# Performance work log

Measured on AMD Instinct MI355X. Metric: run time of the kernel, lower is better.

## Reference

```python
import jax, jax.numpy as jnp
import numpy as np

H, KVH, D = 32, 8, 128          # query heads, kv heads, head dim
HID = H * D                      # 4096
N_REP = H // KVH
HEAVY_RATIO, RECENT_RATIO = 0.1, 0.1
B, S = 1, 2048


def setup_inputs() -> dict:
    key = jax.random.key(0)
    ks = jax.random.split(key, 8)
    scale = 0.02
    hidden_states = jax.random.normal(ks[0], (B, S, HID), jnp.float32)
    neg = jnp.finfo(jnp.float32).min
    causal = jnp.where(jnp.tril(jnp.ones((S, S), bool)), 0.0, neg)
    attention_mask = jnp.broadcast_to(causal[None, None], (B, 1, S, S)).astype(jnp.float32)
    return {
        "hidden_states": hidden_states,
        "attention_mask": attention_mask,
        "Wq": jax.random.normal(ks[1], (HID, H * D), jnp.float32) * scale,
        "bq": jax.random.normal(ks[2], (H * D,), jnp.float32) * scale,
        "Wk": jax.random.normal(ks[3], (HID, KVH * D), jnp.float32) * scale,
        "bk": jax.random.normal(ks[4], (KVH * D,), jnp.float32) * scale,
        "Wv": jax.random.normal(ks[5], (HID, KVH * D), jnp.float32) * scale,
        "bv": jax.random.normal(ks[6], (KVH * D,), jnp.float32) * scale,
        "Wo": jax.random.normal(ks[7], (H * D, HID), jnp.float32) * scale,
    }


def reference(hidden_states, attention_mask, Wq, bq, Wk, bk, Wv, bv, Wo):
    b, s, _ = hidden_states.shape
    # QKV projections (q/k/v have bias, o does not)
    q = (hidden_states @ Wq + bq).reshape(b, s, H, D).transpose(0, 2, 1, 3)      # [B,H,S,D]
    k = (hidden_states @ Wk + bk).reshape(b, s, KVH, D).transpose(0, 2, 1, 3)    # [B,KVH,S,D]
    v = (hidden_states @ Wv + bv).reshape(b, s, KVH, D).transpose(0, 2, 1, 3)
    # repeat_kv: head h uses kv head h // N_REP (matches expand+reshape order)
    k = jnp.repeat(k, N_REP, axis=1)                                             # [B,H,S,D]
    v = jnp.repeat(v, N_REP, axis=1)
    scores = jnp.einsum('bhqd,bhkd->bhqk', q, k) / jnp.sqrt(jnp.asarray(D, q.dtype))
    neg = jnp.finfo(scores.dtype).min
    scores = jnp.maximum(scores + attention_mask, neg)
    attn = jax.nn.softmax(scores.astype(jnp.float32), axis=-1).astype(q.dtype)   # [B,H,S,S]
    # H2O: accumulate per-key scores (first step: no previous_scores)
    cur_scores = attn.sum(axis=0).sum(axis=1)                                    # [H, S]
    heavy_budget = int(HEAVY_RATIO * s)
    recent_budget = int(RECENT_RATIO * s)
    # cache_budget = heavy + recent < s, so eviction branch always runs here
    mask = jnp.ones((H, s + 1), attn.dtype)
    mask = mask.at[:, : s + 1 - recent_budget].set(0.0)
    selected = cur_scores[:, : s - recent_budget]                                # exclude recent window
    _, topk_idx = jax.lax.top_k(selected, heavy_budget)                          # [H, heavy]
    mask = jax.vmap(lambda m, i: m.at[i].set(1.0))(mask, topk_idx)               # scatter heavy hitters
    attention_masks_next = mask[None, :, None, :]                                # [1,H,1,S+1]
    score_mask = mask[:, :-1].at[:, -recent_budget:].set(1.0)
    new_scores = cur_scores * score_mask                                         # evicted scores zeroed
    # attention output
    out = jnp.einsum('bhqk,bhkd->bhqd', attn, v)                                 # [B,H,S,D]
    out = out.transpose(0, 2, 1, 3).reshape(b, s, HID) @ Wo
    return out, attention_masks_next, new_scores
```

## Files before the change

### kernel.cpp

```cpp
#include <hip/hip_runtime.h>
#include <stdint.h>

#define SEQ 2048
#define HID 4096
#define KVHID 1024
#define NHEAD 32
#define DHEAD 128
#define HEAVY 204
#define SEL_N 1844

typedef float f32x4 __attribute__((ext_vector_type(4)));
typedef __bf16 bf16x8 __attribute__((ext_vector_type(8)));

#define MFMA16 __builtin_amdgcn_mfma_f32_16x16x32_bf16

__device__ __forceinline__ unsigned short f2bf(float x) {
    unsigned int u = __float_as_uint(x);
    u = (u + 0x7fffu + ((u >> 16) & 1u)) >> 16;
    return (unsigned short)u;
}
__device__ __forceinline__ float bf2f(unsigned short s) {
    return __uint_as_float(((unsigned int)s) << 16);
}
__device__ __forceinline__ unsigned long long pack4(unsigned short a, unsigned short b,
                                                    unsigned short c, unsigned short d) {
    return (unsigned long long)a | ((unsigned long long)b << 16) |
           ((unsigned long long)c << 32) | ((unsigned long long)d << 48);
}
__device__ __forceinline__ float fexp2(float x) {
#if __has_builtin(__builtin_amdgcn_exp2f)
    return __builtin_amdgcn_exp2f(x);
#else
    float r; asm volatile("v_exp_f32 %0, %1\ns_nop 1" : "=v"(r) : "v"(x)); return r;
#endif
}
__device__ __forceinline__ unsigned cvt_pk_bf16(float lo, float hi) {
    unsigned r; asm("v_cvt_pk_bf16_f32 %0, %1, %2" : "=v"(r) : "v"(lo), "v"(hi)); return r;
}
__device__ __forceinline__ void gload_lds16(const unsigned short* g, unsigned short* l) {
    __builtin_amdgcn_global_load_lds(
        (const __attribute__((address_space(1))) void*)g,
        (__attribute__((address_space(3))) void*)l, 16, 0, 0);
}
__device__ __forceinline__ void block_sync() {
    asm volatile("" ::: "memory");
    __builtin_amdgcn_s_barrier();
    asm volatile("" ::: "memory");
}

__global__ __launch_bounds__(256) void split_f32(const float* __restrict__ in,
    unsigned short* __restrict__ hi, unsigned short* __restrict__ lo, int n4)
{
    int i = blockIdx.x * 256 + threadIdx.x;
    const int stride = gridDim.x * 256;
    for (; i < n4; i += stride) {
        const float4 v = ((const float4*)in)[i];
        const unsigned short h0 = f2bf(v.x), h1 = f2bf(v.y), h2 = f2bf(v.z), h3 = f2bf(v.w);
        ((unsigned long long*)hi)[i] = pack4(h0, h1, h2, h3);
        ((unsigned long long*)lo)[i] = pack4(f2bf(v.x - bf2f(h0)), f2bf(v.y - bf2f(h1)),
                                             f2bf(v.z - bf2f(h2)), f2bf(v.w - bf2f(h3)));
    }
}

template<bool SPLIT>
__global__ __launch_bounds__(256) void wprep(const float* __restrict__ W,
    unsigned short* __restrict__ Thi, unsigned short* __restrict__ Tlo, int K, int N)
{
    __shared__ float T[64][65];
    const int k0 = blockIdx.y << 6, n0 = blockIdx.x << 6;
    const int tid = threadIdx.x;
    const int c = tid & 63, r4 = tid >> 6;
    #pragma unroll
    for (int i = 0; i < 16; ++i)
        T[r4 + i * 4][c] = W[(size_t)(k0 + r4 + i * 4) * N + n0 + c];
    __syncthreads();
    #pragma unroll
    for (int i = 0; i < 16; ++i) {
        const int n = r4 + i * 4;
        const float x = T[c][n];
        const size_t o = (size_t)(n0 + n) * K + k0 + c;
        const unsigned short h = f2bf(x);
        Thi[o] = h;
        if constexpr (SPLIT) Tlo[o] = f2bf(x - bf2f(h));
    }
}

template<bool SPLIT, int OUTMODE , bool BIAS>
__global__ __launch_bounds__(256) void gemm2(
    const unsigned short* __restrict__ Ahi, const unsigned short* __restrict__ Alo,
    const unsigned short* __restrict__ Bhi, const unsigned short* __restrict__ Blo,
    const float* __restrict__ bias,
    void* __restrict__ C0, unsigned short* __restrict__ C1,
    int M, int N, int K)
{
    constexpr int NT = SPLIT ? 4 : 2;
    __shared__ unsigned short sm[2][NT][128 * 32];

    const int tid = threadIdx.x;
    const int l = tid & 63, w = tid >> 6;
    const int lr = l & 15, lg = l >> 4;
    const int wm = (w >> 1) * 64, wn = (w & 1) * 64;
    const int m0 = blockIdx.y * 128, n0 = blockIdx.x * 128;

    const unsigned short* aH = Ahi + (size_t)m0 * K;
    const unsigned short* bH = Bhi + (size_t)n0 * K;
    const unsigned short* aL = SPLIT ? Alo + (size_t)m0 * K : nullptr;
    const unsigned short* bL = SPLIT ? Blo + (size_t)n0 * K : nullptr;

    const int s0_ = tid, s1_ = tid + 256;
    const int r0_ = s0_ >> 2, c0_ = (s0_ & 3) ^ (r0_ & 3);
    const int r1_ = s1_ >> 2, c1_ = (s1_ & 3) ^ (r1_ & 3);
    const size_t g0off = (size_t)r0_ * K + c0_ * 8;
    const size_t g1off = (size_t)r1_ * K + c1_ * 8;

#define STAGE(buf, kk)                                                          \
    do {                                                                        \
        const int k0s = (kk) << 5;                                              \
        gload_lds16(aH + g0off + k0s, &sm[buf][0][s0_ * 8]);                    \
        gload_lds16(aH + g1off + k0s, &sm[buf][0][s1_ * 8]);                    \
        gload_lds16(bH + g0off + k0s, &sm[buf][1][s0_ * 8]);                    \
        gload_lds16(bH + g1off + k0s, &sm[buf][1][s1_ * 8]);                    \
        if constexpr (SPLIT) {                                                  \
            gload_lds16(aL + g0off + k0s, &sm[buf][2][s0_ * 8]);                \
            gload_lds16(aL + g1off + k0s, &sm[buf][2][s1_ * 8]);                \
            gload_lds16(bL + g0off + k0s, &sm[buf][3][s0_ * 8]);                \
            gload_lds16(bL + g1off + k0s, &sm[buf][3][s1_ * 8]);                \
        }                                                                       \
    } while (0)

    f32x4 acc[4][4];
    #pragma unroll
    for (int i = 0; i < 4; ++i)
        #pragma unroll
        for (int j = 0; j < 4; ++j) acc[i][j] = (f32x4){};

    const int nk = K >> 5;
    STAGE(0, 0);
    for (int kt = 0; kt < nk; ++kt) {
        if (kt + 1 < nk) {
            STAGE((kt + 1) & 1, kt + 1);
            if constexpr (SPLIT) asm volatile("s_waitcnt vmcnt(8)" ::: "memory");
            else                 asm volatile("s_waitcnt vmcnt(4)" ::: "memory");
        } else {
            asm volatile("s_waitcnt vmcnt(0)" ::: "memory");
        }
        block_sync();
        {
            const unsigned short (*smb)[128 * 32] = sm[kt & 1];
            bf16x8 ah[4], bh[4], al[4], bl[4];
            #pragma unroll
            for (int mi = 0; mi < 4; ++mi) {
                const int rr = wm + mi * 16 + lr;
                const int o = rr * 32 + ((lg ^ (rr & 3)) << 3);
                ah[mi] = *(const bf16x8*)(&smb[0][o]);
                if constexpr (SPLIT) al[mi] = *(const bf16x8*)(&smb[2][o]);
            }
            #pragma unroll
            for (int ni = 0; ni < 4; ++ni) {
                const int rr = wn + ni * 16 + lr;
                const int o = rr * 32 + ((lg ^ (rr & 3)) << 3);
                bh[ni] = *(const bf16x8*)(&smb[1][o]);
                if constexpr (SPLIT) bl[ni] = *(const bf16x8*)(&smb[3][o]);
            }
            #pragma unroll
            for (int mi = 0; mi < 4; ++mi)
                #pragma unroll
                for (int ni = 0; ni < 4; ++ni) {
                    acc[mi][ni] = MFMA16(ah[mi], bh[ni], acc[mi][ni], 0, 0, 0);
                    if constexpr (SPLIT) {
                        acc[mi][ni] = MFMA16(ah[mi], bl[ni], acc[mi][ni], 0, 0, 0);
                        acc[mi][ni] = MFMA16(al[mi], bh[ni], acc[mi][ni], 0, 0, 0);
                    }
                }
        }
        block_sync();
    }
#undef STAGE

    #pragma unroll
    for (int ni = 0; ni < 4; ++ni) {
        const int col = n0 + wn + ni * 16 + lr;
        float bv = 0.f;
        if constexpr (BIAS) bv = bias[col];
        #pragma unroll
        for (int mi = 0; mi < 4; ++mi) {
            #pragma unroll
            for (int r = 0; r < 4; ++r) {
                const int row = m0 + wm + mi * 16 + lg * 4 + r;
                const float x = acc[mi][ni][r] + bv;
                const size_t o = (size_t)row * N + col;
                if constexpr (OUTMODE == 1) {
                    ((float*)C0)[o] = x;
                } else if constexpr (OUTMODE == 0) {
                    ((unsigned short*)C0)[o] = f2bf(x);
                } else {
                    const unsigned short hi = f2bf(x);
                    ((unsigned short*)C0)[o] = hi;
                    C1[o] = f2bf(x - bf2f(hi));
                }
            }
        }
    }
}

__global__ __launch_bounds__(256) void transpose_v(const unsigned short* __restrict__ v,
                                                   unsigned short* __restrict__ vt)
{
    __shared__ unsigned short T[64][65];
    const int r0 = blockIdx.x * 64;
    const int c0 = blockIdx.y * 64;
    const int tid = threadIdx.x;
    const int cc = tid & 63, rr = tid >> 6;
    #pragma unroll
    for (int i = 0; i < 16; ++i)
        T[rr + i * 4][cc] = v[(size_t)(r0 + rr + i * 4) * KVHID + c0 + cc];
    __syncthreads();
    #pragma unroll
    for (int i = 0; i < 16; ++i) {
        const int oc = rr + i * 4;
        vt[(size_t)(c0 + oc) * SEQ + r0 + cc] = T[cc][oc];
    }
}

__device__ __forceinline__ void stage_tile(
    const unsigned short* __restrict__ khi, const unsigned short* __restrict__ klo,
    unsigned short* kb, int kt, int kvoff, int w, int lane)
{
    const unsigned short* src = (w >> 1) ? klo : khi;
    unsigned short* dst = kb + (w >> 1) * 4096 + (w & 1) * 2048;
    const int lsub = lane >> 4;
    const int lbyte = (lane & 15) * 16;
    #pragma unroll
    for (int j = 0; j < 4; ++j) {
        const int row = (w & 1) * 16 + j * 4 + lsub;
        const int soff = (lbyte ^ ((row & 7) << 4)) >> 1;
        const unsigned short* g = src + (size_t)(kt * 32 + row) * KVHID + kvoff + soff;
        gload_lds16(g, dst + j * 512);
    }
}

__device__ __forceinline__ void process_qblock(
    int head, int qb, int w, int lane,
    const unsigned short* __restrict__ qhi, const unsigned short* __restrict__ qlo,
    const unsigned short* __restrict__ khi, const unsigned short* __restrict__ klo,
    const unsigned short* __restrict__ vT,
    unsigned short* __restrict__ obuf, double* __restrict__ colsum,
    unsigned short* kbuf, unsigned short* pl)
{
    const int lr = lane & 15, lg = lane >> 4;
    const int kv = head >> 2;
    const int kvoff = kv * DHEAD;
    const int q0 = qb * 64;
    const int q0w = q0 + w * 16;
    const int NT = 2 * qb + 2;
    const int wnt = ((q0w + 15) >> 5) + 1;
    const float C = 0.08838834764831845f * 1.44269504088896340f;

    bf16x8 qh[4], qlo4[4];
    {
        const size_t qbase = (size_t)(q0w + lr) * HID + head * DHEAD + lg * 8;
        #pragma unroll
        for (int s = 0; s < 4; ++s) {
            qh[s]   = *(const bf16x8*)(qhi + qbase + s * 32);
            qlo4[s] = *(const bf16x8*)(qlo + qbase + s * 32);
        }
    }
    const int swz = (lr & 7) << 3;

    float rl[4];
    {
        float lp[4] = {0.f, 0.f, 0.f, 0.f};
        stage_tile(khi, klo, kbuf, 0, kvoff, w, lane);
        for (int kt = 0; kt < NT; ++kt) {
            unsigned short* kb = kbuf + (kt & 1) * 8192;
            if (kt + 1 < NT) {
                stage_tile(khi, klo, kbuf + ((kt + 1) & 1) * 8192, kt + 1, kvoff, w, lane);
                asm volatile("s_waitcnt vmcnt(4)" ::: "memory");
            } else {
                asm volatile("s_waitcnt vmcnt(0)" ::: "memory");
            }
            block_sync();
            if (kt < wnt) {
                f32x4 m0 = {}, m1 = {}, x0 = {}, x1 = {};
                #pragma unroll
                for (int s = 0; s < 4; ++s) {
                    const int d = s * 32 + lg * 8;
                    const bf16x8 k0h = *(const bf16x8*)(kb + (lr * 128 + (d ^ swz)));
                    const bf16x8 k1h = *(const bf16x8*)(kb + ((16 + lr) * 128 + (d ^ swz)));
                    const bf16x8 k0l = *(const bf16x8*)(kb + 4096 + lr * 128 + (d ^ swz));
                    const bf16x8 k1l = *(const bf16x8*)(kb + 4096 + (16 + lr) * 128 + (d ^ swz));
                    m0 = MFMA16(qh[s], k0h, m0, 0, 0, 0);
                    m1 = MFMA16(qh[s], k1h, m1, 0, 0, 0);
                    x0 = MFMA16(qlo4[s], k0h, MFMA16(qh[s], k0l, x0, 0, 0, 0), 0, 0, 0);
                    x1 = MFMA16(qlo4[s], k1h, MFMA16(qh[s], k1l, x1, 0, 0, 0), 0, 0, 0);
                }
                const bool full = (kt * 32 + 31 <= q0w);
                #pragma unroll
                for (int r = 0; r < 4; ++r) {
                    float e0 = fexp2((m0[r] + x0[r]) * C);
                    float e1 = fexp2((m1[r] + x1[r]) * C);
                    if (!full) {
                        const int q = q0w + lg * 4 + r;
                        if (kt * 32 + lr > q)      e0 = 0.f;
                        if (kt * 32 + 16 + lr > q) e1 = 0.f;
                    }
                    lp[r] += e0 + e1;
                }
            }
            block_sync();
        }
        #pragma unroll
        for (int r = 0; r < 4; ++r) {
            float v = lp[r];
            v += __shfl_xor(v, 1);
            v += __shfl_xor(v, 2);
            v += __shfl_xor(v, 4);
            v += __shfl_xor(v, 8);
            rl[r] = 1.0f / v;
        }
    }
    {
        f32x4 oacc[8];
        #pragma unroll
        for (int f = 0; f < 8; ++f) oacc[f] = (f32x4){};
        stage_tile(khi, klo, kbuf, 0, kvoff, w, lane);
        for (int kt = 0; kt < NT; ++kt) {
            unsigned short* kb = kbuf + (kt & 1) * 8192;
            if (kt + 1 < NT) {
                stage_tile(khi, klo, kbuf + ((kt + 1) & 1) * 8192, kt + 1, kvoff, w, lane);
                asm volatile("s_waitcnt vmcnt(4)" ::: "memory");
            } else {
                asm volatile("s_waitcnt vmcnt(0)" ::: "memory");
            }
            block_sync();
            if (kt < wnt) {
                f32x4 m0 = {}, m1 = {}, x0 = {}, x1 = {};
                #pragma unroll
                for (int s = 0; s < 4; ++s) {
                    const int d = s * 32 + lg * 8;
                    const bf16x8 k0h = *(const bf16x8*)(kb + (lr * 128 + (d ^ swz)));
                    const bf16x8 k1h = *(const bf16x8*)(kb + ((16 + lr) * 128 + (d ^ swz)));
                    const bf16x8 k0l = *(const bf16x8*)(kb + 4096 + lr * 128 + (d ^ swz));
                    const bf16x8 k1l = *(const bf16x8*)(kb + 4096 + (16 + lr) * 128 + (d ^ swz));
                    m0 = MFMA16(qh[s], k0h, m0, 0, 0, 0);
                    m1 = MFMA16(qh[s], k1h, m1, 0, 0, 0);
                    x0 = MFMA16(qlo4[s], k0h, MFMA16(qh[s], k0l, x0, 0, 0, 0), 0, 0, 0);
                    x1 = MFMA16(qlo4[s], k1h, MFMA16(qh[s], k1l, x1, 0, 0, 0), 0, 0, 0);
                }
                const bool full = (kt * 32 + 31 <= q0w);
                float p0[4], p1[4];
                float cs0 = 0.f, cs1 = 0.f;
                #pragma unroll
                for (int r = 0; r < 4; ++r) {
                    float e0 = fexp2((m0[r] + x0[r]) * C);
                    float e1 = fexp2((m1[r] + x1[r]) * C);
                    if (!full) {
                        const int q = q0w + lg * 4 + r;
                        if (kt * 32 + lr > q)      e0 = 0.f;
                        if (kt * 32 + 16 + lr > q) e1 = 0.f;
                    }
                    p0[r] = e0 * rl[r];
                    p1[r] = e1 * rl[r];
                    cs0 += p0[r];
                    cs1 += p1[r];
                }
                cs0 += __shfl_xor(cs0, 16); cs0 += __shfl_xor(cs0, 32);
                cs1 += __shfl_xor(cs1, 16); cs1 += __shfl_xor(cs1, 32);
                if (lg == 0) {
                    atomicAdd(&colsum[head * SEQ + kt * 32 + lr], (double)cs0);
                    atomicAdd(&colsum[head * SEQ + kt * 32 + 16 + lr], (double)cs1);
                }
                #pragma unroll
                for (int r = 0; r < 4; r += 2) {
                    const int row0 = (lg * 4 + r) * 40;
                    unsigned u0 = cvt_pk_bf16(p0[r], p0[r + 1]);
                    unsigned u1 = cvt_pk_bf16(p1[r], p1[r + 1]);
                    pl[row0 + lr]      = (unsigned short)u0;
                    pl[row0 + 40 + lr] = (unsigned short)(u0 >> 16);
                    pl[row0 + 16 + lr] = (unsigned short)u1;
                    pl[row0 + 56 + lr] = (unsigned short)(u1 >> 16);
                }
                const bf16x8 pa = *(const bf16x8*)(pl + lr * 40 + lg * 8);
                #pragma unroll
                for (int f = 0; f < 8; ++f) {
                    const bf16x8 vf = *(const bf16x8*)(vT + (size_t)(kvoff + f * 16 + lr) * SEQ
                                                       + kt * 32 + lg * 8);
                    oacc[f] = MFMA16(pa, vf, oacc[f], 0, 0, 0);
                }
            }
            block_sync();
        }
        #pragma unroll
        for (int f = 0; f < 8; ++f)
            #pragma unroll
            for (int r = 0; r < 4; ++r)
                obuf[(size_t)(q0w + lg * 4 + r) * HID + head * DHEAD + f * 16 + lr] =
                    f2bf(oacc[f][r]);
    }
}

__global__ __launch_bounds__(256, 2) void attn_fused2(
    const unsigned short* __restrict__ qhi, const unsigned short* __restrict__ qlo,
    const unsigned short* __restrict__ khi, const unsigned short* __restrict__ klo,
    const unsigned short* __restrict__ vT,
    unsigned short* __restrict__ obuf, double* __restrict__ colsum)
{
    __shared__ unsigned short kbuf[2][2 * 4096];
    __shared__ unsigned short plds[4][16 * 40];
    const int head = blockIdx.x >> 4;
    const int pr = blockIdx.x & 15;
    const int tid = threadIdx.x;
    const int w = tid >> 6, lane = tid & 63;
    process_qblock(head, pr, w, lane, qhi, qlo, khi, klo, vT, obuf, colsum,
                   &kbuf[0][0], &plds[w][0]);
    process_qblock(head, 31 - pr, w, lane, qhi, qlo, khi, klo, vT, obuf, colsum,
                   &kbuf[0][0], &plds[w][0]);
}

__global__ __launch_bounds__(256) void topk_kernel(const double* __restrict__ colsum,
                                                   float* __restrict__ outbuf)
{
    __shared__ float sc[SEL_N];
    __shared__ unsigned char fl[SEL_N];
    __shared__ int cnt;
    const int h = blockIdx.x;
    const int tid = threadIdx.x;
    for (int j = tid; j < SEL_N; j += 256) {
        sc[j] = (float)colsum[h * SEQ + j];
        fl[j] = 0;
    }
    __syncthreads();
    unsigned int cand = 0u;
    for (int b = 30; b >= 0; --b) {
        const unsigned int t = cand | (1u << b);
        const float tv = __uint_as_float(t);
        if (tid == 0) cnt = 0;
        __syncthreads();
        int local = 0;
        for (int j = tid; j < SEL_N; j += 256) local += (sc[j] >= tv) ? 1 : 0;
        atomicAdd(&cnt, local);
        __syncthreads();
        if (cnt >= HEAVY) cand = t;
        __syncthreads();
    }
    const float v204 = __uint_as_float(cand);
    if (tid == 0) cnt = 0;
    __syncthreads();
    int local = 0;
    for (int j = tid; j < SEL_N; j += 256) {
        if (sc[j] > v204) { fl[j] = 1; local++; }
    }
    atomicAdd(&cnt, local);
    __syncthreads();
    if (tid == 0) {
        int need = HEAVY - cnt;
        for (int j = 0; j < SEL_N && need > 0; ++j) {
            if (sc[j] == v204) { fl[j] = 1; --need; }
        }
    }
    __syncthreads();
    float* mask_out = outbuf + 8388608 + h * 2049;
    float* score_out = outbuf + 8388608 + NHEAD * 2049 + h * SEQ;
    for (int j = tid; j < 2049; j += 256) {
        float mv;
        if (j >= 1845) mv = 1.f;
        else if (j < SEL_N) mv = fl[j] ? 1.f : 0.f;
        else mv = 0.f;
        mask_out[j] = mv;
    }
    for (int j = tid; j < SEQ; j += 256) {
        const float cur = (float)colsum[h * SEQ + j];
        const float smv = (j >= SEL_N) ? 1.f : (fl[j] ? 1.f : 0.f);
        score_out[j] = cur * smv;
    }
}

extern "C" void kernel_launch(void* const* d_in, const int* in_sizes, int n_in,
                              void* d_out, int out_size, void* d_ws, size_t ws_size,
                              hipStream_t stream)
{
    const float* hidden = (const float*)d_in[0];
    const float* Wq = (const float*)d_in[2];
    const float* bq = (const float*)d_in[3];
    const float* Wk = (const float*)d_in[4];
    const float* bk = (const float*)d_in[5];
    const float* Wv = (const float*)d_in[6];
    const float* bv = (const float*)d_in[7];
    const float* Wo = (const float*)d_in[8];
    float* out = (float*)d_out;

    char* ws = (char*)d_ws;
    unsigned short* hs_hi = (unsigned short*)(ws);
    unsigned short* hs_lo = (unsigned short*)(ws + 16777216ull);
    unsigned short* wqT_hi = (unsigned short*)(ws + 33554432ull);
    unsigned short* wqT_lo = (unsigned short*)(ws + 67108864ull);
    unsigned short* wkT_hi = (unsigned short*)(ws + 100663296ull);
    unsigned short* wkT_lo = (unsigned short*)(ws + 109051904ull);
    unsigned short* wvT    = (unsigned short*)(ws + 117440512ull);
    unsigned short* q_hi   = (unsigned short*)(ws + 125829120ull);
    unsigned short* q_lo   = (unsigned short*)(ws + 142606336ull);
    unsigned short* k_hi   = (unsigned short*)(ws + 159383552ull);
    unsigned short* k_lo   = (unsigned short*)(ws + 163577856ull);
    unsigned short* v_bf   = (unsigned short*)(ws + 167772160ull);
    unsigned short* vT     = (unsigned short*)(ws + 171966464ull);
    unsigned short* o_bf   = (unsigned short*)(ws + 176160768ull);
    double* colsum         = (double*)(ws + 192937984ull);
    unsigned short* woT    = wqT_hi;

    dim3 blk(256);
    split_f32<<<dim3(2048), blk, 0, stream>>>(hidden, hs_hi, hs_lo, (SEQ * HID) / 4);
    wprep<true><<<dim3(64, 64), blk, 0, stream>>>(Wq, wqT_hi, wqT_lo, HID, HID);
    wprep<true><<<dim3(16, 64), blk, 0, stream>>>(Wk, wkT_hi, wkT_lo, HID, KVHID);
    wprep<false><<<dim3(16, 64), blk, 0, stream>>>(Wv, wvT, nullptr, HID, KVHID);

    gemm2<true, 2, true><<<dim3(32, 16), blk, 0, stream>>>(
        hs_hi, hs_lo, wqT_hi, wqT_lo, bq, q_hi, q_lo, SEQ, HID, HID);
    gemm2<true, 2, true><<<dim3(8, 16), blk, 0, stream>>>(
        hs_hi, hs_lo, wkT_hi, wkT_lo, bk, k_hi, k_lo, SEQ, KVHID, HID);
    gemm2<false, 0, true><<<dim3(8, 16), blk, 0, stream>>>(
        hs_hi, nullptr, wvT, nullptr, bv, v_bf, nullptr, SEQ, KVHID, HID);

    transpose_v<<<dim3(32, 16), blk, 0, stream>>>(v_bf, vT);
    (void)hipMemsetAsync((void*)colsum, 0, (size_t)NHEAD * SEQ * sizeof(double), stream);
    attn_fused2<<<dim3(512), blk, 0, stream>>>(q_hi, q_lo, k_hi, k_lo, vT, o_bf, colsum);
    topk_kernel<<<dim3(32), blk, 0, stream>>>(colsum, out);

    wprep<false><<<dim3(64, 64), blk, 0, stream>>>(Wo, woT, nullptr, HID, HID);
    gemm2<false, 1, false><<<dim3(32, 16), blk, 0, stream>>>(
        o_bf, nullptr, woT, nullptr, nullptr, out, nullptr, SEQ, HID, HID);
}
```

Measured before the change: 855.3 us.

## Split attention into one block per q-block with scrambled order and MFMA priority

The attention kernel now launches 1024 blocks, one per (head, q-block), instead of 512 blocks that each processed a paired short and long causal q-block. A hashed q-block index spreads work across CUs, and launch bounds are raised to 4 blocks per CU for higher occupancy. It also breaks the dependent MFMA chains for the hi/lo correction terms into independent accumulators and wraps MFMA sections (including the GEMM) in s_setprio. The cost is losing the explicit causal load-pairing and adding register pressure under the tighter launch bound.

```diff
diff --git a/kernel.cpp b/kernel.cpp
--- a/kernel.cpp
+++ b/kernel.cpp
@@ -162,6 +162,7 @@
                 bh[ni] = *(const bf16x8*)(&smb[1][o]);
                 if constexpr (SPLIT) bl[ni] = *(const bf16x8*)(&smb[3][o]);
             }
+            __builtin_amdgcn_s_setprio(1);
             #pragma unroll
             for (int mi = 0; mi < 4; ++mi)
                 #pragma unroll
@@ -172,6 +173,7 @@
                         acc[mi][ni] = MFMA16(al[mi], bh[ni], acc[mi][ni], 0, 0, 0);
                     }
                 }
+            __builtin_amdgcn_s_setprio(0);
         }
         block_sync();
     }
@@ -239,19 +241,23 @@
     }
 }
 
-__device__ __forceinline__ void process_qblock(
-    int head, int qb, int w, int lane,
+__global__ __launch_bounds__(256, 4) void attn_fused3(
     const unsigned short* __restrict__ qhi, const unsigned short* __restrict__ qlo,
     const unsigned short* __restrict__ khi, const unsigned short* __restrict__ klo,
     const unsigned short* __restrict__ vT,
-    unsigned short* __restrict__ obuf, double* __restrict__ colsum,
-    unsigned short* kbuf, unsigned short* pl)
-{
+    unsigned short* __restrict__ obuf, double* __restrict__ colsum)
+{
+    __shared__ unsigned short kbuf[2][2 * 4096];
+    __shared__ unsigned short plds[4][16 * 40];
+    const int head = blockIdx.x >> 5;
+    const int qb = ((blockIdx.x & 31) * 13 + head * 7) & 31;
+    const int tid = threadIdx.x;
+    const int w = tid >> 6, lane = tid & 63;
+    unsigned short* pl = &plds[w][0];
+
     const int lr = lane & 15, lg = lane >> 4;
-    const int kv = head >> 2;
-    const int kvoff = kv * DHEAD;
-    const int q0 = qb * 64;
-    const int q0w = q0 + w * 16;
+    const int kvoff = (head >> 2) * DHEAD;
+    const int q0w = qb * 64 + w * 16;
     const int NT = 2 * qb + 2;
     const int wnt = ((q0w + 15) >> 5) + 1;
     const float C = 0.08838834764831845f * 1.44269504088896340f;
@@ -270,18 +276,19 @@
     float rl[4];
     {
         float lp[4] = {0.f, 0.f, 0.f, 0.f};
-        stage_tile(khi, klo, kbuf, 0, kvoff, w, lane);
+        stage_tile(khi, klo, &kbuf[0][0], 0, kvoff, w, lane);
         for (int kt = 0; kt < NT; ++kt) {
-            unsigned short* kb = kbuf + (kt & 1) * 8192;
+            unsigned short* kb = &kbuf[kt & 1][0];
             if (kt + 1 < NT) {
-                stage_tile(khi, klo, kbuf + ((kt + 1) & 1) * 8192, kt + 1, kvoff, w, lane);
+                stage_tile(khi, klo, &kbuf[(kt + 1) & 1][0], kt + 1, kvoff, w, lane);
                 asm volatile("s_waitcnt vmcnt(4)" ::: "memory");
             } else {
                 asm volatile("s_waitcnt vmcnt(0)" ::: "memory");
             }
             block_sync();
             if (kt < wnt) {
-                f32x4 m0 = {}, m1 = {}, x0 = {}, x1 = {};
+                f32x4 m0 = {}, m1 = {}, xa0 = {}, xb0 = {}, xa1 = {}, xb1 = {};
+                __builtin_amdgcn_s_setprio(1);
                 #pragma unroll
                 for (int s = 0; s < 4; ++s) {
                     const int d = s * 32 + lg * 8;
@@ -289,16 +296,19 @@
                     const bf16x8 k1h = *(const bf16x8*)(kb + ((16 + lr) * 128 + (d ^ swz)));
                     const bf16x8 k0l = *(const bf16x8*)(kb + 4096 + lr * 128 + (d ^ swz));
                     const bf16x8 k1l = *(const bf16x8*)(kb + 4096 + (16 + lr) * 128 + (d ^ swz));
-                    m0 = MFMA16(qh[s], k0h, m0, 0, 0, 0);
-                    m1 = MFMA16(qh[s], k1h, m1, 0, 0, 0);
-                    x0 = MFMA16(qlo4[s], k0h, MFMA16(qh[s], k0l, x0, 0, 0, 0), 0, 0, 0);
-                    x1 = MFMA16(qlo4[s], k1h, MFMA16(qh[s], k1l, x1, 0, 0, 0), 0, 0, 0);
-                }
+                    m0  = MFMA16(qh[s],   k0h, m0,  0, 0, 0);
+                    m1  = MFMA16(qh[s],   k1h, m1,  0, 0, 0);
+                    xa0 = MFMA16(qh[s],   k0l, xa0, 0, 0, 0);
+                    xb0 = MFMA16(qlo4[s], k0h, xb0, 0, 0, 0);
+                    xa1 = MFMA16(qh[s],   k1l, xa1, 0, 0, 0);
+                    xb1 = MFMA16(qlo4[s], k1h, xb1, 0, 0, 0);
+                }
+                __builtin_amdgcn_s_setprio(0);
                 const bool full = (kt * 32 + 31 <= q0w);
                 #pragma unroll
                 for (int r = 0; r < 4; ++r) {
-                    float e0 = fexp2((m0[r] + x0[r]) * C);
-                    float e1 = fexp2((m1[r] + x1[r]) * C);
+                    float e0 = fexp2((m0[r] + (xa0[r] + xb0[r])) * C);
+                    float e1 = fexp2((m1[r] + (xa1[r] + xb1[r])) * C);
                     if (!full) {
                         const int q = q0w + lg * 4 + r;
                         if (kt * 32 + lr > q)      e0 = 0.f;
@@ -323,18 +333,19 @@
         f32x4 oacc[8];
         #pragma unroll
         for (int f = 0; f < 8; ++f) oacc[f] = (f32x4){};
-        stage_tile(khi, klo, kbuf, 0, kvoff, w, lane);
+        stage_tile(khi, klo, &kbuf[0][0], 0, kvoff, w, lane);
         for (int kt = 0; kt < NT; ++kt) {
-            unsigned short* kb = kbuf + (kt & 1) * 8192;
+            unsigned short* kb = &kbuf[kt & 1][0];
             if (kt + 1 < NT) {
-                stage_tile(khi, klo, kbuf + ((kt + 1) & 1) * 8192, kt + 1, kvoff, w, lane);
+                stage_tile(khi, klo, &kbuf[(kt + 1) & 1][0], kt + 1, kvoff, w, lane);
                 asm volatile("s_waitcnt vmcnt(4)" ::: "memory");
             } else {
                 asm volatile("s_waitcnt vmcnt(0)" ::: "memory");
             }
             block_sync();
             if (kt < wnt) {
-                f32x4 m0 = {}, m1 = {}, x0 = {}, x1 = {};
+                f32x4 m0 = {}, m1 = {}, xa0 = {}, xb0 = {}, xa1 = {}, xb1 = {};
+                __builtin_amdgcn_s_setprio(1);
                 #pragma unroll
                 for (int s = 0; s < 4; ++s) {
                     const int d = s * 32 + lg * 8;
@@ -342,18 +353,21 @@
                     const bf16x8 k1h = *(const bf16x8*)(kb + ((16 + lr) * 128 + (d ^ swz)));
                     const bf16x8 k0l = *(const bf16x8*)(kb + 4096 + lr * 128 + (d ^ swz));
                     const bf16x8 k1l = *(const bf16x8*)(kb + 4096 + (16 + lr) * 128 + (d ^ swz));
-                    m0 = MFMA16(qh[s], k0h, m0, 0, 0, 0);
-                    m1 = MFMA16(qh[s], k1h, m1, 0, 0, 0);
-                    x0 = MFMA16(qlo4[s], k0h, MFMA16(qh[s], k0l, x0, 0, 0, 0), 0, 0, 0);
-                    x1 = MFMA16(qlo4[s], k1h, MFMA16(qh[s], k1l, x1, 0, 0, 0), 0, 0, 0);
-                }
+                    m0  = MFMA16(qh[s],   k0h, m0,  0, 0, 0);
+                    m1  = MFMA16(qh[s],   k1h, m1,  0, 0, 0);
+                    xa0 = MFMA16(qh[s],   k0l, xa0, 0, 0, 0);
+                    xb0 = MFMA16(qlo4[s], k0h, xb0, 0, 0, 0);
+                    xa1 = MFMA16(qh[s],   k1l, xa1, 0, 0, 0);
+                    xb1 = MFMA16(qlo4[s], k1h, xb1, 0, 0, 0);
+                }
+                __builtin_amdgcn_s_setprio(0);
                 const bool full = (kt * 32 + 31 <= q0w);
                 float p0[4], p1[4];
                 float cs0 = 0.f, cs1 = 0.f;
                 #pragma unroll
                 for (int r = 0; r < 4; ++r) {
-                    float e0 = fexp2((m0[r] + x0[r]) * C);
-                    float e1 = fexp2((m1[r] + x1[r]) * C);
+                    float e0 = fexp2((m0[r] + (xa0[r] + xb0[r])) * C);
+                    float e1 = fexp2((m1[r] + (xa1[r] + xb1[r])) * C);
                     if (!full) {
                         const int q = q0w + lg * 4 + r;
                         if (kt * 32 + lr > q)      e0 = 0.f;
@@ -381,12 +395,14 @@
                     pl[row0 + 56 + lr] = (unsigned short)(u1 >> 16);
                 }
                 const bf16x8 pa = *(const bf16x8*)(pl + lr * 40 + lg * 8);
+                __builtin_amdgcn_s_setprio(1);
                 #pragma unroll
                 for (int f = 0; f < 8; ++f) {
                     const bf16x8 vf = *(const bf16x8*)(vT + (size_t)(kvoff + f * 16 + lr) * SEQ
                                                        + kt * 32 + lg * 8);
                     oacc[f] = MFMA16(pa, vf, oacc[f], 0, 0, 0);
                 }
+                __builtin_amdgcn_s_setprio(0);
             }
             block_sync();
         }
@@ -397,24 +413,6 @@
                 obuf[(size_t)(q0w + lg * 4 + r) * HID + head * DHEAD + f * 16 + lr] =
                     f2bf(oacc[f][r]);
     }
-}
-
-__global__ __launch_bounds__(256, 2) void attn_fused2(
-    const unsigned short* __restrict__ qhi, const unsigned short* __restrict__ qlo,
-    const unsigned short* __restrict__ khi, const unsigned short* __restrict__ klo,
-    const unsigned short* __restrict__ vT,
-    unsigned short* __restrict__ obuf, double* __restrict__ colsum)
-{
-    __shared__ unsigned short kbuf[2][2 * 4096];
-    __shared__ unsigned short plds[4][16 * 40];
-    const int head = blockIdx.x >> 4;
-    const int pr = blockIdx.x & 15;
-    const int tid = threadIdx.x;
-    const int w = tid >> 6, lane = tid & 63;
-    process_qblock(head, pr, w, lane, qhi, qlo, khi, klo, vT, obuf, colsum,
-                   &kbuf[0][0], &plds[w][0]);
-    process_qblock(head, 31 - pr, w, lane, qhi, qlo, khi, klo, vT, obuf, colsum,
-                   &kbuf[0][0], &plds[w][0]);
 }
 
 __global__ __launch_bounds__(256) void topk_kernel(const double* __restrict__ colsum,
@@ -522,7 +520,7 @@
 
     transpose_v<<<dim3(32, 16), blk, 0, stream>>>(v_bf, vT);
     (void)hipMemsetAsync((void*)colsum, 0, (size_t)NHEAD * SEQ * sizeof(double), stream);
-    attn_fused2<<<dim3(512), blk, 0, stream>>>(q_hi, q_lo, k_hi, k_lo, vT, o_bf, colsum);
+    attn_fused3<<<dim3(1024), blk, 0, stream>>>(q_hi, q_lo, k_hi, k_lo, vT, o_bf, colsum);
     topk_kernel<<<dim3(32), blk, 0, stream>>>(colsum, out);
 
     wprep<false><<<dim3(64, 64), blk, 0, stream>>>(Wo, woT, nullptr, HID, HID);
```

After: 1.029 ms. 20.3% more time.

## Split attention into one block per q-block with alternating order, pad P LDS, raise MFMA priority

Applied to the files above, without the earlier changes.

The attention kernel now launches one block per (head, q-block), 1024 blocks instead of 512 blocks that each handled a paired short and long q-block. The block-to-work mapping alternates ascending and descending q-block order across groups of eight heads to balance the causal workload. The P staging buffer row stride moves from 40 to 44 elements to reduce LDS bank conflicts. The GEMM inner loop also raises wave priority around its MFMA burst. More, smaller blocks give finer load balancing but lose the guaranteed short/long pairing inside each block.

```diff
diff --git a/kernel.cpp b/kernel.cpp
--- a/kernel.cpp
+++ b/kernel.cpp
@@ -162,6 +162,7 @@
                 bh[ni] = *(const bf16x8*)(&smb[1][o]);
                 if constexpr (SPLIT) bl[ni] = *(const bf16x8*)(&smb[3][o]);
             }
+            __builtin_amdgcn_s_setprio(1);
             #pragma unroll
             for (int mi = 0; mi < 4; ++mi)
                 #pragma unroll
@@ -172,6 +173,7 @@
                         acc[mi][ni] = MFMA16(al[mi], bh[ni], acc[mi][ni], 0, 0, 0);
                     }
                 }
+            __builtin_amdgcn_s_setprio(0);
         }
         block_sync();
     }
@@ -239,19 +241,26 @@
     }
 }
 
-__device__ __forceinline__ void process_qblock(
-    int head, int qb, int w, int lane,
+__global__ __launch_bounds__(256, 2) void attn_fused5(
     const unsigned short* __restrict__ qhi, const unsigned short* __restrict__ qlo,
     const unsigned short* __restrict__ khi, const unsigned short* __restrict__ klo,
     const unsigned short* __restrict__ vT,
-    unsigned short* __restrict__ obuf, double* __restrict__ colsum,
-    unsigned short* kbuf, unsigned short* pl)
-{
+    unsigned short* __restrict__ obuf, double* __restrict__ colsum)
+{
+    __shared__ unsigned short kbuf[2][2 * 4096];
+    __shared__ unsigned short plds[4][16 * 44];
+    const int i = blockIdx.x;
+    const int u = i & 255;
+    const int s_ = i >> 8;
+    const int head = (u >> 5) + (s_ << 3);
+    const int qb = (s_ & 1) ? (31 - (u & 31)) : (u & 31);
+    const int tid = threadIdx.x;
+    const int w = tid >> 6, lane = tid & 63;
+    unsigned short* pl = &plds[w][0];
+
     const int lr = lane & 15, lg = lane >> 4;
-    const int kv = head >> 2;
-    const int kvoff = kv * DHEAD;
-    const int q0 = qb * 64;
-    const int q0w = q0 + w * 16;
+    const int kvoff = (head >> 2) * DHEAD;
+    const int q0w = qb * 64 + w * 16;
     const int NT = 2 * qb + 2;
     const int wnt = ((q0w + 15) >> 5) + 1;
     const float C = 0.08838834764831845f * 1.44269504088896340f;
@@ -270,11 +279,11 @@
     float rl[4];
     {
         float lp[4] = {0.f, 0.f, 0.f, 0.f};
-        stage_tile(khi, klo, kbuf, 0, kvoff, w, lane);
+        stage_tile(khi, klo, &kbuf[0][0], 0, kvoff, w, lane);
         for (int kt = 0; kt < NT; ++kt) {
-            unsigned short* kb = kbuf + (kt & 1) * 8192;
+            unsigned short* kb = &kbuf[kt & 1][0];
             if (kt + 1 < NT) {
-                stage_tile(khi, klo, kbuf + ((kt + 1) & 1) * 8192, kt + 1, kvoff, w, lane);
+                stage_tile(khi, klo, &kbuf[(kt + 1) & 1][0], kt + 1, kvoff, w, lane);
                 asm volatile("s_waitcnt vmcnt(4)" ::: "memory");
             } else {
                 asm volatile("s_waitcnt vmcnt(0)" ::: "memory");
@@ -323,11 +332,11 @@
         f32x4 oacc[8];
         #pragma unroll
         for (int f = 0; f < 8; ++f) oacc[f] = (f32x4){};
-        stage_tile(khi, klo, kbuf, 0, kvoff, w, lane);
+        stage_tile(khi, klo, &kbuf[0][0], 0, kvoff, w, lane);
         for (int kt = 0; kt < NT; ++kt) {
-            unsigned short* kb = kbuf + (kt & 1) * 8192;
+            unsigned short* kb = &kbuf[kt & 1][0];
             if (kt + 1 < NT) {
-                stage_tile(khi, klo, kbuf + ((kt + 1) & 1) * 8192, kt + 1, kvoff, w, lane);
+                stage_tile(khi, klo, &kbuf[(kt + 1) & 1][0], kt + 1, kvoff, w, lane);
                 asm volatile("s_waitcnt vmcnt(4)" ::: "memory");
             } else {
                 asm volatile("s_waitcnt vmcnt(0)" ::: "memory");
@@ -372,15 +381,15 @@
                 }
                 #pragma unroll
                 for (int r = 0; r < 4; r += 2) {
-                    const int row0 = (lg * 4 + r) * 40;
+                    const int row0 = (lg * 4 + r) * 44;
                     unsigned u0 = cvt_pk_bf16(p0[r], p0[r + 1]);
                     unsigned u1 = cvt_pk_bf16(p1[r], p1[r + 1]);
                     pl[row0 + lr]      = (unsigned short)u0;
-                    pl[row0 + 40 + lr] = (unsigned short)(u0 >> 16);
+                    pl[row0 + 44 + lr] = (unsigned short)(u0 >> 16);
                     pl[row0 + 16 + lr] = (unsigned short)u1;
-                    pl[row0 + 56 + lr] = (unsigned short)(u1 >> 16);
-                }
-                const bf16x8 pa = *(const bf16x8*)(pl + lr * 40 + lg * 8);
+                    pl[row0 + 60 + lr] = (unsigned short)(u1 >> 16);
+                }
+                const bf16x8 pa = *(const bf16x8*)(pl + lr * 44 + lg * 8);
                 #pragma unroll
                 for (int f = 0; f < 8; ++f) {
                     const bf16x8 vf = *(const bf16x8*)(vT + (size_t)(kvoff + f * 16 + lr) * SEQ
@@ -397,24 +406,6 @@
                 obuf[(size_t)(q0w + lg * 4 + r) * HID + head * DHEAD + f * 16 + lr] =
                     f2bf(oacc[f][r]);
     }
-}
-
-__global__ __launch_bounds__(256, 2) void attn_fused2(
-    const unsigned short* __restrict__ qhi, const unsigned short* __restrict__ qlo,
-    const unsigned short* __restrict__ khi, const unsigned short* __restrict__ klo,
-    const unsigned short* __restrict__ vT,
-    unsigned short* __restrict__ obuf, double* __restrict__ colsum)
-{
-    __shared__ unsigned short kbuf[2][2 * 4096];
-    __shared__ unsigned short plds[4][16 * 40];
-    const int head = blockIdx.x >> 4;
-    const int pr = blockIdx.x & 15;
-    const int tid = threadIdx.x;
-    const int w = tid >> 6, lane = tid & 63;
-    process_qblock(head, pr, w, lane, qhi, qlo, khi, klo, vT, obuf, colsum,
-                   &kbuf[0][0], &plds[w][0]);
-    process_qblock(head, 31 - pr, w, lane, qhi, qlo, khi, klo, vT, obuf, colsum,
-                   &kbuf[0][0], &plds[w][0]);
 }
 
 __global__ __launch_bounds__(256) void topk_kernel(const double* __restrict__ colsum,
@@ -522,7 +513,7 @@
 
     transpose_v<<<dim3(32, 16), blk, 0, stream>>>(v_bf, vT);
     (void)hipMemsetAsync((void*)colsum, 0, (size_t)NHEAD * SEQ * sizeof(double), stream);
-    attn_fused2<<<dim3(512), blk, 0, stream>>>(q_hi, q_lo, k_hi, k_lo, vT, o_bf, colsum);
+    attn_fused5<<<dim3(1024), blk, 0, stream>>>(q_hi, q_lo, k_hi, k_lo, vT, o_bf, colsum);
     topk_kernel<<<dim3(32), blk, 0, stream>>>(colsum, out);
 
     wprep<false><<<dim3(64, 64), blk, 0, stream>>>(Wo, woT, nullptr, HID, HID);
```

Result: slower. 927.3 us (+8.4%).

## Split attention into row-sum and PV kernels with key-tile halves across blocks

Applied to the files above, without the earlier changes.

The fused attention kernel becomes two kernels, each launching twice as many blocks. Each block handles alternate key tiles (even or odd) of a query-block pair. The first pass atomically accumulates softmax denominators into a float buffer. The second pass computes normalized probabilities, column sums and partial PV outputs into two fp32 buffers, which a merge kernel adds and converts to bf16. It also raises wave priority around the GEMM MFMA block. The aim is more parallelism in the attention stage, at the cost of extra launches, fp32 partial-output traffic, float atomics for the row sums, and reused workspace regions.

```diff
diff --git a/kernel.cpp b/kernel.cpp
--- a/kernel.cpp
+++ b/kernel.cpp
@@ -162,6 +162,7 @@
                 bh[ni] = *(const bf16x8*)(&smb[1][o]);
                 if constexpr (SPLIT) bl[ni] = *(const bf16x8*)(&smb[3][o]);
             }
+            __builtin_amdgcn_s_setprio(1);
             #pragma unroll
             for (int mi = 0; mi < 4; ++mi)
                 #pragma unroll
@@ -172,6 +173,7 @@
                         acc[mi][ni] = MFMA16(al[mi], bh[ni], acc[mi][ni], 0, 0, 0);
                     }
                 }
+            __builtin_amdgcn_s_setprio(0);
         }
         block_sync();
     }
@@ -239,19 +241,15 @@
     }
 }
 
-__device__ __forceinline__ void process_qblock(
-    int head, int qb, int w, int lane,
+__device__ __forceinline__ void qblock_sumA(
+    int head, int qb, int h, int w, int lane,
     const unsigned short* __restrict__ qhi, const unsigned short* __restrict__ qlo,
     const unsigned short* __restrict__ khi, const unsigned short* __restrict__ klo,
-    const unsigned short* __restrict__ vT,
-    unsigned short* __restrict__ obuf, double* __restrict__ colsum,
-    unsigned short* kbuf, unsigned short* pl)
+    float* __restrict__ lbuf, unsigned short* kbuf)
 {
     const int lr = lane & 15, lg = lane >> 4;
-    const int kv = head >> 2;
-    const int kvoff = kv * DHEAD;
-    const int q0 = qb * 64;
-    const int q0w = q0 + w * 16;
+    const int kvoff = (head >> 2) * DHEAD;
+    const int q0w = qb * 64 + w * 16;
     const int NT = 2 * qb + 2;
     const int wnt = ((q0w + 15) >> 5) + 1;
     const float C = 0.08838834764831845f * 1.44269504088896340f;
@@ -267,154 +265,213 @@
     }
     const int swz = (lr & 7) << 3;
 
-    float rl[4];
-    {
-        float lp[4] = {0.f, 0.f, 0.f, 0.f};
-        stage_tile(khi, klo, kbuf, 0, kvoff, w, lane);
-        for (int kt = 0; kt < NT; ++kt) {
-            unsigned short* kb = kbuf + (kt & 1) * 8192;
-            if (kt + 1 < NT) {
-                stage_tile(khi, klo, kbuf + ((kt + 1) & 1) * 8192, kt + 1, kvoff, w, lane);
-                asm volatile("s_waitcnt vmcnt(4)" ::: "memory");
-            } else {
-                asm volatile("s_waitcnt vmcnt(0)" ::: "memory");
-            }
-            block_sync();
-            if (kt < wnt) {
-                f32x4 m0 = {}, m1 = {}, x0 = {}, x1 = {};
-                #pragma unroll
-                for (int s = 0; s < 4; ++s) {
-                    const int d = s * 32 + lg * 8;
-                    const bf16x8 k0h = *(const bf16x8*)(kb + (lr * 128 + (d ^ swz)));
-                    const bf16x8 k1h = *(const bf16x8*)(kb + ((16 + lr) * 128 + (d ^ swz)));
-                    const bf16x8 k0l = *(const bf16x8*)(kb + 4096 + lr * 128 + (d ^ swz));
-                    const bf16x8 k1l = *(const bf16x8*)(kb + 4096 + (16 + lr) * 128 + (d ^ swz));
-                    m0 = MFMA16(qh[s], k0h, m0, 0, 0, 0);
-                    m1 = MFMA16(qh[s], k1h, m1, 0, 0, 0);
-                    x0 = MFMA16(qlo4[s], k0h, MFMA16(qh[s], k0l, x0, 0, 0, 0), 0, 0, 0);
-                    x1 = MFMA16(qlo4[s], k1h, MFMA16(qh[s], k1l, x1, 0, 0, 0), 0, 0, 0);
+    float lp[4] = {0.f, 0.f, 0.f, 0.f};
+    stage_tile(khi, klo, kbuf, h, kvoff, w, lane);
+    for (int kt = h; kt < NT; kt += 2) {
+        unsigned short* kb = kbuf + ((kt >> 1) & 1) * 8192;
+        if (kt + 2 < NT) {
+            stage_tile(khi, klo, kbuf + (((kt >> 1) + 1) & 1) * 8192, kt + 2, kvoff, w, lane);
+            asm volatile("s_waitcnt vmcnt(4)" ::: "memory");
+        } else {
+            asm volatile("s_waitcnt vmcnt(0)" ::: "memory");
+        }
+        block_sync();
+        if (kt < wnt) {
+            f32x4 m0 = {}, m1 = {}, x0 = {}, x1 = {};
+            #pragma unroll
+            for (int s = 0; s < 4; ++s) {
+                const int d = s * 32 + lg * 8;
+                const bf16x8 k0h = *(const bf16x8*)(kb + (lr * 128 + (d ^ swz)));
+                const bf16x8 k1h = *(const bf16x8*)(kb + ((16 + lr) * 128 + (d ^ swz)));
+                const bf16x8 k0l = *(const bf16x8*)(kb + 4096 + lr * 128 + (d ^ swz));
+                const bf16x8 k1l = *(const bf16x8*)(kb + 4096 + (16 + lr) * 128 + (d ^ swz));
+                m0 = MFMA16(qh[s], k0h, m0, 0, 0, 0);
+                m1 = MFMA16(qh[s], k1h, m1, 0, 0, 0);
+                x0 = MFMA16(qlo4[s], k0h, MFMA16(qh[s], k0l, x0, 0, 0, 0), 0, 0, 0);
+                x1 = MFMA16(qlo4[s], k1h, MFMA16(qh[s], k1l, x1, 0, 0, 0), 0, 0, 0);
+            }
+            const bool full = (kt * 32 + 31 <= q0w);
+            #pragma unroll
+            for (int r = 0; r < 4; ++r) {
+                float e0 = fexp2((m0[r] + x0[r]) * C);
+                float e1 = fexp2((m1[r] + x1[r]) * C);
+                if (!full) {
+                    const int q = q0w + lg * 4 + r;
+                    if (kt * 32 + lr > q)      e0 = 0.f;
+                    if (kt * 32 + 16 + lr > q) e1 = 0.f;
                 }
-                const bool full = (kt * 32 + 31 <= q0w);
-                #pragma unroll
-                for (int r = 0; r < 4; ++r) {
-                    float e0 = fexp2((m0[r] + x0[r]) * C);
-                    float e1 = fexp2((m1[r] + x1[r]) * C);
-                    if (!full) {
-                        const int q = q0w + lg * 4 + r;
-                        if (kt * 32 + lr > q)      e0 = 0.f;
-                        if (kt * 32 + 16 + lr > q) e1 = 0.f;
-                    }
-                    lp[r] += e0 + e1;
-                }
-            }
-            block_sync();
-        }
-        #pragma unroll
-        for (int r = 0; r < 4; ++r) {
-            float v = lp[r];
-            v += __shfl_xor(v, 1);
-            v += __shfl_xor(v, 2);
-            v += __shfl_xor(v, 4);
-            v += __shfl_xor(v, 8);
-            rl[r] = 1.0f / v;
-        }
-    }
-    {
-        f32x4 oacc[8];
-        #pragma unroll
-        for (int f = 0; f < 8; ++f) oacc[f] = (f32x4){};
-        stage_tile(khi, klo, kbuf, 0, kvoff, w, lane);
-        for (int kt = 0; kt < NT; ++kt) {
-            unsigned short* kb = kbuf + (kt & 1) * 8192;
-            if (kt + 1 < NT) {
-                stage_tile(khi, klo, kbuf + ((kt + 1) & 1) * 8192, kt + 1, kvoff, w, lane);
-                asm volatile("s_waitcnt vmcnt(4)" ::: "memory");
-            } else {
-                asm volatile("s_waitcnt vmcnt(0)" ::: "memory");
-            }
-            block_sync();
-            if (kt < wnt) {
-                f32x4 m0 = {}, m1 = {}, x0 = {}, x1 = {};
-                #pragma unroll
-                for (int s = 0; s < 4; ++s) {
-                    const int d = s * 32 + lg * 8;
-                    const bf16x8 k0h = *(const bf16x8*)(kb + (lr * 128 + (d ^ swz)));
-                    const bf16x8 k1h = *(const bf16x8*)(kb + ((16 + lr) * 128 + (d ^ swz)));
-                    const bf16x8 k0l = *(const bf16x8*)(kb + 4096 + lr * 128 + (d ^ swz));
-                    const bf16x8 k1l = *(const bf16x8*)(kb + 4096 + (16 + lr) * 128 + (d ^ swz));
-                    m0 = MFMA16(qh[s], k0h, m0, 0, 0, 0);
-                    m1 = MFMA16(qh[s], k1h, m1, 0, 0, 0);
-                    x0 = MFMA16(qlo4[s], k0h, MFMA16(qh[s], k0l, x0, 0, 0, 0), 0, 0, 0);
-                    x1 = MFMA16(qlo4[s], k1h, MFMA16(qh[s], k1l, x1, 0, 0, 0), 0, 0, 0);
-                }
-                const bool full = (kt * 32 + 31 <= q0w);
-                float p0[4], p1[4];
-                float cs0 = 0.f, cs1 = 0.f;
-                #pragma unroll
-                for (int r = 0; r < 4; ++r) {
-                    float e0 = fexp2((m0[r] + x0[r]) * C);
-                    float e1 = fexp2((m1[r] + x1[r]) * C);
-                    if (!full) {
-                        const int q = q0w + lg * 4 + r;
-                        if (kt * 32 + lr > q)      e0 = 0.f;
-                        if (kt * 32 + 16 + lr > q) e1 = 0.f;
-                    }
-                    p0[r] = e0 * rl[r];
-                    p1[r] = e1 * rl[r];
-                    cs0 += p0[r];
-                    cs1 += p1[r];
-                }
-                cs0 += __shfl_xor(cs0, 16); cs0 += __shfl_xor(cs0, 32);
-                cs1 += __shfl_xor(cs1, 16); cs1 += __shfl_xor(cs1, 32);
-                if (lg == 0) {
-                    atomicAdd(&colsum[head * SEQ + kt * 32 + lr], (double)cs0);
-                    atomicAdd(&colsum[head * SEQ + kt * 32 + 16 + lr], (double)cs1);
-                }
-                #pragma unroll
-                for (int r = 0; r < 4; r += 2) {
-                    const int row0 = (lg * 4 + r) * 40;
-                    unsigned u0 = cvt_pk_bf16(p0[r], p0[r + 1]);
-                    unsigned u1 = cvt_pk_bf16(p1[r], p1[r + 1]);
-                    pl[row0 + lr]      = (unsigned short)u0;
-                    pl[row0 + 40 + lr] = (unsigned short)(u0 >> 16);
-                    pl[row0 + 16 + lr] = (unsigned short)u1;
-                    pl[row0 + 56 + lr] = (unsigned short)(u1 >> 16);
-                }
-                const bf16x8 pa = *(const bf16x8*)(pl + lr * 40 + lg * 8);
-                #pragma unroll
-                for (int f = 0; f < 8; ++f) {
-                    const bf16x8 vf = *(const bf16x8*)(vT + (size_t)(kvoff + f * 16 + lr) * SEQ
-                                                       + kt * 32 + lg * 8);
-                    oacc[f] = MFMA16(pa, vf, oacc[f], 0, 0, 0);
-                }
-            }
-            block_sync();
-        }
-        #pragma unroll
-        for (int f = 0; f < 8; ++f)
-            #pragma unroll
-            for (int r = 0; r < 4; ++r)
-                obuf[(size_t)(q0w + lg * 4 + r) * HID + head * DHEAD + f * 16 + lr] =
-                    f2bf(oacc[f][r]);
-    }
-}
-
-__global__ __launch_bounds__(256, 2) void attn_fused2(
+                lp[r] += e0 + e1;
+            }
+        }
+        block_sync();
+    }
+    #pragma unroll
+    for (int r = 0; r < 4; ++r) {
+        float v = lp[r];
+        v += __shfl_xor(v, 1);
+        v += __shfl_xor(v, 2);
+        v += __shfl_xor(v, 4);
+        v += __shfl_xor(v, 8);
+        if (lr == 0) atomicAdd(&lbuf[head * SEQ + q0w + lg * 4 + r], v);
+    }
+}
+
+__global__ __launch_bounds__(256, 2) void attn_sumA(
     const unsigned short* __restrict__ qhi, const unsigned short* __restrict__ qlo,
     const unsigned short* __restrict__ khi, const unsigned short* __restrict__ klo,
-    const unsigned short* __restrict__ vT,
-    unsigned short* __restrict__ obuf, double* __restrict__ colsum)
+    float* __restrict__ lbuf)
+{
+    __shared__ unsigned short kbuf[2][2 * 4096];
+    const int id = blockIdx.x;
+    const int head = id >> 5;
+    const int pr = (id & 31) >> 1;
+    const int h = id & 1;
+    const int tid = threadIdx.x;
+    const int w = tid >> 6, lane = tid & 63;
+    qblock_sumA(head, pr, h, w, lane, qhi, qlo, khi, klo, lbuf, &kbuf[0][0]);
+    qblock_sumA(head, 31 - pr, h, w, lane, qhi, qlo, khi, klo, lbuf, &kbuf[0][0]);
+}
+
+__device__ __forceinline__ void qblock_pvB(
+    int head, int qb, int h, int w, int lane,
+    const unsigned short* __restrict__ qhi, const unsigned short* __restrict__ qlo,
+    const unsigned short* __restrict__ khi, const unsigned short* __restrict__ klo,
+    const unsigned short* __restrict__ vT, const float* __restrict__ lbuf,
+    float* __restrict__ o32, double* __restrict__ colsum,
+    unsigned short* kbuf, unsigned short* pl)
+{
+    const int lr = lane & 15, lg = lane >> 4;
+    const int kvoff = (head >> 2) * DHEAD;
+    const int q0w = qb * 64 + w * 16;
+    const int NT = 2 * qb + 2;
+    const int wnt = ((q0w + 15) >> 5) + 1;
+    const float C = 0.08838834764831845f * 1.44269504088896340f;
+
+    bf16x8 qh[4], qlo4[4];
+    {
+        const size_t qbase = (size_t)(q0w + lr) * HID + head * DHEAD + lg * 8;
+        #pragma unroll
+        for (int s = 0; s < 4; ++s) {
+            qh[s]   = *(const bf16x8*)(qhi + qbase + s * 32);
+            qlo4[s] = *(const bf16x8*)(qlo + qbase + s * 32);
+        }
+    }
+    const int swz = (lr & 7) << 3;
+
+    float rl[4];
+    #pragma unroll
+    for (int r = 0; r < 4; ++r)
+        rl[r] = 1.0f / lbuf[head * SEQ + q0w + lg * 4 + r];
+
+    f32x4 oacc[8];
+    #pragma unroll
+    for (int f = 0; f < 8; ++f) oacc[f] = (f32x4){};
+    stage_tile(khi, klo, kbuf, h, kvoff, w, lane);
+    for (int kt = h; kt < NT; kt += 2) {
+        unsigned short* kb = kbuf + ((kt >> 1) & 1) * 8192;
+        if (kt + 2 < NT) {
+            stage_tile(khi, klo, kbuf + (((kt >> 1) + 1) & 1) * 8192, kt + 2, kvoff, w, lane);
+            asm volatile("s_waitcnt vmcnt(4)" ::: "memory");
+        } else {
+            asm volatile("s_waitcnt vmcnt(0)" ::: "memory");
+        }
+        block_sync();
+        if (kt < wnt) {
+            f32x4 m0 = {}, m1 = {}, x0 = {}, x1 = {};
+            #pragma unroll
+            for (int s = 0; s < 4; ++s) {
+                const int d = s * 32 + lg * 8;
+                const bf16x8 k0h = *(const bf16x8*)(kb + (lr * 128 + (d ^ swz)));
+                const bf16x8 k1h = *(const bf16x8*)(kb + ((16 + lr) * 128 + (d ^ swz)));
+                const bf16x8 k0l = *(const bf16x8*)(kb + 4096 + lr * 128 + (d ^ swz));
+                const bf16x8 k1l = *(const bf16x8*)(kb + 4096 + (16 + lr) * 128 + (d ^ swz));
+                m0 = MFMA16(qh[s], k0h, m0, 0, 0, 0);
+                m1 = MFMA16(qh[s], k1h, m1, 0, 0, 0);
+                x0 = MFMA16(qlo4[s], k0h, MFMA16(qh[s], k0l, x0, 0, 0, 0), 0, 0, 0);
+                x1 = MFMA16(qlo4[s], k1h, MFMA16(qh[s], k1l, x1, 0, 0, 0), 0, 0, 0);
+            }
+            const bool full = (kt * 32 + 31 <= q0w);
+            float p0[4], p1[4];
+            float cs0 = 0.f, cs1 = 0.f;
+            #pragma unroll
+            for (int r = 0; r < 4; ++r) {
+                float e0 = fexp2((m0[r] + x0[r]) * C);
+                float e1 = fexp2((m1[r] + x1[r]) * C);
+                if (!full) {
+                    const int q = q0w + lg * 4 + r;
+                    if (kt * 32 + lr > q)      e0 = 0.f;
+                    if (kt * 32 + 16 + lr > q) e1 = 0.f;
+                }
+                p0[r] = e0 * rl[r];
+                p1[r] = e1 * rl[r];
+                cs0 += p0[r];
+                cs1 += p1[r];
+            }
+            cs0 += __shfl_xor(cs0, 16); cs0 += __shfl_xor(cs0, 32);
+            cs1 += __shfl_xor(cs1, 16); cs1 += __shfl_xor(cs1, 32);
+            if (lg == 0) {
+                atomicAdd(&colsum[head * SEQ + kt * 32 + lr], (double)cs0);
+                atomicAdd(&colsum[head * SEQ + kt * 32 + 16 + lr], (double)cs1);
+            }
+            #pragma unroll
+            for (int r = 0; r < 4; r += 2) {
+                const int row0 = (lg * 4 + r) * 40;
+                unsigned u0 = cvt_pk_bf16(p0[r], p0[r + 1]);
+                unsigned u1 = cvt_pk_bf16(p1[r], p1[r + 1]);
+                pl[row0 + lr]      = (unsigned short)u0;
+                pl[row0 + 40 + lr] = (unsigned short)(u0 >> 16);
+                pl[row0 + 16 + lr] = (unsigned short)u1;
+                pl[row0 + 56 + lr] = (unsigned short)(u1 >> 16);
+            }
+            const bf16x8 pa = *(const bf16x8*)(pl + lr * 40 + lg * 8);
+            #pragma unroll
+            for (int f = 0; f < 8; ++f) {
+                const bf16x8 vf = *(const bf16x8*)(vT + (size_t)(kvoff + f * 16 + lr) * SEQ
+                                                   + kt * 32 + lg * 8);
+                oacc[f] = MFMA16(pa, vf, oacc[f], 0, 0, 0);
+            }
+        }
+        block_sync();
+    }
+    #pragma unroll
+    for (int f = 0; f < 8; ++f)
+        #pragma unroll
+        for (int r = 0; r < 4; ++r)
+            o32[(size_t)(q0w + lg * 4 + r) * HID + head * DHEAD + f * 16 + lr] = oacc[f][r];
+}
+
+__global__ __launch_bounds__(256, 2) void attn_pvB(
+    const unsigned short* __restrict__ qhi, const unsigned short* __restrict__ qlo,
+    const unsigned short* __restrict__ khi, const unsigned short* __restrict__ klo,
+    const unsigned short* __restrict__ vT, const float* __restrict__ lbuf,
+    float* __restrict__ o32a, float* __restrict__ o32b, double* __restrict__ colsum)
 {
     __shared__ unsigned short kbuf[2][2 * 4096];
     __shared__ unsigned short plds[4][16 * 40];
-    const int head = blockIdx.x >> 4;
-    const int pr = blockIdx.x & 15;
+    const int id = blockIdx.x;
+    const int head = id >> 5;
+    const int pr = (id & 31) >> 1;
+    const int h = id & 1;
     const int tid = threadIdx.x;
     const int w = tid >> 6, lane = tid & 63;
-    process_qblock(head, pr, w, lane, qhi, qlo, khi, klo, vT, obuf, colsum,
-                   &kbuf[0][0], &plds[w][0]);
-    process_qblock(head, 31 - pr, w, lane, qhi, qlo, khi, klo, vT, obuf, colsum,
-                   &kbuf[0][0], &plds[w][0]);
+    float* o32 = h ? o32b : o32a;
+    qblock_pvB(head, pr, h, w, lane, qhi, qlo, khi, klo, vT, lbuf, o32, colsum,
+               &kbuf[0][0], &plds[w][0]);
+    qblock_pvB(head, 31 - pr, h, w, lane, qhi, qlo, khi, klo, vT, lbuf, o32, colsum,
+               &kbuf[0][0], &plds[w][0]);
+}
+
+__global__ __launch_bounds__(256) void merge_o(const float* __restrict__ a,
+    const float* __restrict__ b, unsigned short* __restrict__ o, int n4)
+{
+    int i = blockIdx.x * 256 + threadIdx.x;
+    const int stride = gridDim.x * 256;
+    for (; i < n4; i += stride) {
+        const float4 va = ((const float4*)a)[i];
+        const float4 vb = ((const float4*)b)[i];
+        ((unsigned long long*)o)[i] = pack4(f2bf(va.x + vb.x), f2bf(va.y + vb.y),
+                                            f2bf(va.z + vb.z), f2bf(va.w + vb.w));
+    }
 }
 
 __global__ __launch_bounds__(256) void topk_kernel(const double* __restrict__ colsum,
@@ -505,7 +562,10 @@
     unsigned short* vT     = (unsigned short*)(ws + 171966464ull);
     unsigned short* o_bf   = (unsigned short*)(ws + 176160768ull);
     double* colsum         = (double*)(ws + 192937984ull);
+    float* lbuf            = (float*)(ws + 193462272ull);
     unsigned short* woT    = wqT_hi;
+    float* o32a            = (float*)(ws);
+    float* o32b            = (float*)(ws + 67108864ull);
 
     dim3 blk(256);
     split_f32<<<dim3(2048), blk, 0, stream>>>(hidden, hs_hi, hs_lo, (SEQ * HID) / 4);
@@ -521,8 +581,12 @@
         hs_hi, nullptr, wvT, nullptr, bv, v_bf, nullptr, SEQ, KVHID, HID);
 
     transpose_v<<<dim3(32, 16), blk, 0, stream>>>(v_bf, vT);
-    (void)hipMemsetAsync((void*)colsum, 0, (size_t)NHEAD * SEQ * sizeof(double), stream);
-    attn_fused2<<<dim3(512), blk, 0, stream>>>(q_hi, q_lo, k_hi, k_lo, vT, o_bf, colsum);
+    (void)hipMemsetAsync((void*)colsum, 0,
+                         (size_t)NHEAD * SEQ * (sizeof(double) + sizeof(float)), stream);
+    attn_sumA<<<dim3(1024), blk, 0, stream>>>(q_hi, q_lo, k_hi, k_lo, lbuf);
+    attn_pvB<<<dim3(1024), blk, 0, stream>>>(q_hi, q_lo, k_hi, k_lo, vT, lbuf,
+                                             o32a, o32b, colsum);
+    merge_o<<<dim3(2048), blk, 0, stream>>>(o32a, o32b, o_bf, (SEQ * HID) / 4);
     topk_kernel<<<dim3(32), blk, 0, stream>>>(colsum, out);
 
     wprep<false><<<dim3(64, 64), blk, 0, stream>>>(Wo, woT, nullptr, HID, HID);
```

New measurement: 904.6 us. +5.8%, slower.
